# Kernel optimization log

Measured on AMD Instinct MI355X. Metric: run time of the kernel, lower is better.

The kernel has to match this reference:

```python
import jax, jax.numpy as jnp
import numpy as np

CHANNELS = 256
C8 = CHANNELS // 8


def setup_inputs() -> dict:
    key = jax.random.key(0)
    ks = jax.random.split(key, 7)
    b, c, h, w = 4, CHANNELS, 64, 64
    x = jax.random.normal(ks[0], (b, c, h, w), dtype=jnp.float32)
    # 1x1 conv weights stored as [out_ch, in_ch] (kernel is 1x1)
    s = 1.0 / np.sqrt(c)
    wq = jax.random.uniform(ks[1], (C8, c), jnp.float32, -s, s)
    bq = jax.random.uniform(ks[2], (C8,), jnp.float32, -s, s)
    wk = jax.random.uniform(ks[3], (C8, c), jnp.float32, -s, s)
    bk = jax.random.uniform(ks[4], (C8,), jnp.float32, -s, s)
    wv = jax.random.uniform(ks[5], (c, c), jnp.float32, -s, s)
    bv = jax.random.uniform(ks[6], (c,), jnp.float32, -s, s)
    return {"x": x, "wq": wq, "bq": bq, "wk": wk, "bk": bk, "wv": wv, "bv": bv}


def reference(x, wq, bq, wk, bk, wv, bv):
    b, c, h, w = x.shape
    n = h * w
    xf = x.reshape(b, c, n)                                  # (b, c, n)
    q = jnp.einsum('oc,bcn->bon', wq, xf) + bq[None, :, None]  # (b, c/8, n)
    k = jnp.einsum('oc,bcn->bon', wk, xf) + bk[None, :, None]  # (b, c/8, n)
    v = jnp.einsum('oc,bcn->bon', wv, xf) + bv[None, :, None]  # (b, c, n)
    # attention[b, i, j] = softmax_j( q[:, :, i] . k[:, :, j] )
    scores = jnp.einsum('bdi,bdj->bij', q, k)                # (b, n, n)
    attn = jax.nn.softmax(scores, axis=-1)
    # out = value @ attention^T  -> out[b, c, i] = sum_j v[b, c, j] * attn[b, i, j]
    out = jnp.einsum('bcj,bij->bci', v, attn)                # (b, c, n)
    return out.reshape(b, c, h, w) + x
```

## Files before the change

### kernel.cpp

```cpp
#include <hip/hip_runtime.h>
#include <hip/hip_bf16.h>
#include <stdint.h>

#define CH 256
#define D8 32
#define NN 4096

typedef __attribute__((ext_vector_type(8))) short short8;
typedef __attribute__((ext_vector_type(4))) short s16x4;
typedef __attribute__((ext_vector_type(4))) float f32x4;

#define MFMA16(a,b,c) __builtin_amdgcn_mfma_f32_16x16x32_bf16(a,b,c,0,0,0)

static __device__ __forceinline__ short f2bf(float f) {
  union { float f; uint32_t u; } v; v.f = f;
  uint32_t r = v.u + 0x7fffu + ((v.u >> 16) & 1u);
  return (short)(r >> 16);
}
static __device__ __forceinline__ float bf2f(short h) {
  union { float f; uint32_t u; } v; v.u = ((uint32_t)(uint16_t)h) << 16;
  return v.f;
}

__global__ __launch_bounds__(256) void prep_kernel(
    const float* __restrict__ x,
    const float* __restrict__ wq, const float* __restrict__ bq,
    const float* __restrict__ wk, const float* __restrict__ bk,
    const float* __restrict__ wv, const float* __restrict__ bv,
    short* __restrict__ xT, short* __restrict__ WQb,
    short* __restrict__ WKb, short* __restrict__ WVb,
    float* __restrict__ BQ, float* __restrict__ BK, float* __restrict__ BV)
{
  int blk = blockIdx.x, t = threadIdx.x;
  if (blk >= 1024) {
    int idx = (blk - 1024) * 256 + t;
    const float LOG2E = 1.4426950408889634f;
    for (int i = idx; i < D8 * CH; i += 2048) WQb[i] = f2bf(wq[i] * LOG2E);
    for (int i = idx; i < D8 * CH; i += 2048) WKb[i] = f2bf(wk[i]);
    for (int i = idx; i < CH * CH; i += 2048) WVb[i] = f2bf(wv[i]);
    if (idx < D8) { BQ[idx] = bq[idx] * LOG2E; BK[idx] = bk[idx]; }
    if (idx < CH) BV[idx] = bv[idx];
    return;
  }
  int b = blk >> 8, ct = (blk >> 6) & 3, nt = blk & 63;
  __shared__ short T[64][65];
  int j = t & 63, i0 = t >> 6;
  const float* xb = x + ((size_t)b * CH + ct * 64) * NN + nt * 64;
  #pragma unroll
  for (int k = 0; k < 16; ++k) {
    int i = k * 4 + i0;
    T[i][j] = f2bf(xb[(size_t)i * NN + j]);
  }
  __syncthreads();
  short* xTb = xT + ((size_t)b * NN + nt * 64) * CH + ct * 64;
  #pragma unroll
  for (int k = 0; k < 16; ++k) {
    int n = k * 4 + i0;
    xTb[(size_t)n * CH + j] = T[j][n];
  }
}

__global__ __launch_bounds__(256) void proj_kernel(
    const short* __restrict__ xT,
    const short* __restrict__ WQb, const short* __restrict__ WKb,
    const short* __restrict__ WVb,
    const float* __restrict__ BQ, const float* __restrict__ BK,
    const float* __restrict__ BV,
    short* __restrict__ Qh, short* __restrict__ Ql,
    short* __restrict__ Kh, short* __restrict__ Kl,
    short* __restrict__ Vo)
{
  int blk = blockIdx.x, t = threadIdx.x;
  int b = blk >> 8, pt = blk & 255;
  int w = t >> 6, lane = t & 63, g = lane >> 4, lr = lane & 15;
  int p0 = pt * 16;
  __shared__ short Vt[4][16][20];

  const short* xrow = xT + ((size_t)b * NN + p0 + lr) * CH + g * 8;
  short8 a[8];
  #pragma unroll
  for (int s = 0; s < 8; ++s) a[s] = *(const short8*)(xrow + s * 32);

  const f32x4 zf = {0.f, 0.f, 0.f, 0.f};

  #pragma unroll
  for (int i = 0; i < 5; ++i) {
    int tt = w * 5 + i;
    const short* W; const float* Bs; int tloc;
    if (tt < 2)      { W = WQb; Bs = BQ; tloc = tt; }
    else if (tt < 4) { W = WKb; Bs = BK; tloc = tt - 2; }
    else             { W = WVb; Bs = BV; tloc = tt - 4; }
    f32x4 acc = zf;
    #pragma unroll
    for (int s = 0; s < 8; ++s) {
      short8 bb = *(const short8*)(W + (size_t)(tloc * 16 + lr) * CH + s * 32 + g * 8);
      acc = MFMA16(a[s], bb, acc);
    }
    int o = tloc * 16 + lr;
    float bias = Bs[o];
    if (tt < 4) {
      short* Oh = (tt < 2) ? Qh : Kh;
      short* Ol = (tt < 2) ? Ql : Kl;
      #pragma unroll
      for (int r = 0; r < 4; ++r) {
        int pos = p0 + g * 4 + r;
        float val = acc[r] + bias;
        short hi = f2bf(val);
        Oh[((size_t)b * NN + pos) * D8 + o] = hi;
        Ol[((size_t)b * NN + pos) * D8 + o] = f2bf(val - bf2f(hi));
      }
    } else {
      #pragma unroll
      for (int r = 0; r < 4; ++r)
        Vt[w][lr][g * 4 + r] = f2bf(acc[r] + bias);
      int row = lane >> 2, c4 = (lane & 3) * 4;
      s16x4 vv = *(const s16x4*)&Vt[w][row][c4];
      *(s16x4*)(Vo + ((size_t)b * CH + tloc * 16 + row) * NN + p0 + c4) = vv;
    }
  }
}

__global__ __launch_bounds__(512) void attn_kernel(
    const short* __restrict__ Qh, const short* __restrict__ Ql,
    const short* __restrict__ Kh, const short* __restrict__ Kl,
    const short* __restrict__ V, const float* __restrict__ x,
    float* __restrict__ out)
{
  int blk = blockIdx.x, t = threadIdx.x;
  int xcd = blk & 7, idx = blk >> 3;
  int b = xcd >> 1;
  int qt = ((xcd & 1) << 5) + idx;
  int q0 = qt * 64;
  int w = t >> 6, lane = t & 63, g = lane >> 4, lr = lane & 15;
  int wS = w & 3;
  bool isS = (w < 4);
  int cw0 = w * 32;

  union Smem {
    struct {
      short P[2][64 * 64];
      float scale[2][64];
      int   flags[2][4];
    } lp;
    float O[CH][67];
  };
  __shared__ Smem sm;
  __shared__ float l_lds[64];

  const short* Qhb = Qh + (size_t)b * NN * D8;
  const short* Qlb = Ql + (size_t)b * NN * D8;
  const short* Khb = Kh + (size_t)b * NN * D8;
  const short* Klb = Kl + (size_t)b * NN * D8;
  const short* Vb = V + (size_t)b * CH * NN;

  short8 aqh, aql;
  if (isS) {
    aqh = *(const short8*)(Qhb + (size_t)(q0 + wS * 16 + lr) * D8 + g * 8);
    aql = *(const short8*)(Qlb + (size_t)(q0 + wS * 16 + lr) * D8 + g * 8);
  }

  const f32x4 zf = {0.f, 0.f, 0.f, 0.f};
  f32x4 O[4][2];
  #pragma unroll
  for (int i = 0; i < 4; ++i)
    #pragma unroll
    for (int j = 0; j < 2; ++j) O[i][j] = zf;
  float m[4] = {-INFINITY, -INFINITY, -INFINITY, -INFINITY};
  float l[4] = {0.f, 0.f, 0.f, 0.f};

  char* Pbase0 = (char*)&sm.lp.P[0][0];
  char* Pbase1 = (char*)&sm.lp.P[1][0];

#define LOADK(KH, KL, KIDX) do { \
    int _k0 = (KIDX) * 64; \
    _Pragma("unroll") \
    for (int _nt = 0; _nt < 4; ++_nt) { \
      size_t _off = (size_t)(_k0 + _nt * 16 + lr) * D8 + g * 8; \
      KH[_nt] = *(const short8*)(Khb + _off); \
      KL[_nt] = *(const short8*)(Klb + _off); \
    } \
  } while (0)

#define LOADV(VV, KIDX) do { \
    int _k0 = (KIDX) * 64; \
    _Pragma("unroll") \
    for (int _ss = 0; _ss < 2; ++_ss) \
      _Pragma("unroll") \
      for (int _ci = 0; _ci < 2; ++_ci) \
        VV[_ss * 2 + _ci] = *(const short8*)(Vb + \
            (size_t)(cw0 + _ci * 16 + lr) * NN + _k0 + _ss * 32 + g * 8); \
  } while (0)

#define STEP(KB, KH, KL, VV, NKH, NKL, NVV) do { \
    int _buf = (KB) & 1; \
    char* _Pb = _buf ? Pbase1 : Pbase0; \
    int _kn = ((KB) + 1) & 63; \
    if (isS) { \
       \
      f32x4 S[4]; \
      _Pragma("unroll") \
      for (int nt = 0; nt < 4; ++nt) { \
        f32x4 s_ = MFMA16(aql, KH[nt], zf); \
        s_ = MFMA16(aqh, KL[nt], s_); \
        s_ = MFMA16(aqh, KH[nt], s_); \
        S[nt] = s_; \
      } \
      LOADK(NKH, NKL, _kn); \
      LOADV(NVV, _kn); \
       \
      float sc[4]; \
      bool upd = false; \
      _Pragma("unroll") \
      for (int r = 0; r < 4; ++r) { \
        float v = fmaxf(fmaxf(S[0][r], S[1][r]), fmaxf(S[2][r], S[3][r])); \
        v = fmaxf(v, __shfl_xor(v, 1)); \
        v = fmaxf(v, __shfl_xor(v, 2)); \
        v = fmaxf(v, __shfl_xor(v, 4)); \
        v = fmaxf(v, __shfl_xor(v, 8)); \
        bool u = v > m[r] + 8.0f;                 \
        upd |= u; \
        float mn = u ? v : m[r]; \
        sc[r] = __builtin_amdgcn_exp2f(m[r] - mn); \
        m[r] = mn; \
      } \
      bool anyupd = __any((int)upd); \
      float rsum[4] = {0.f, 0.f, 0.f, 0.f}; \
      short pb[4][4]; \
      _Pragma("unroll") \
      for (int nt = 0; nt < 4; ++nt) \
        _Pragma("unroll") \
        for (int r = 0; r < 4; ++r) { \
          float p = __builtin_amdgcn_exp2f(S[nt][r] - m[r]); \
          rsum[r] += p; \
          pb[nt][r] = f2bf(p); \
        } \
      _Pragma("unroll") \
      for (int r = 0; r < 4; ++r) { \
        float v = rsum[r]; \
        v += __shfl_xor(v, 1); v += __shfl_xor(v, 2); \
        v += __shfl_xor(v, 4); v += __shfl_xor(v, 8); \
        l[r] = l[r] * sc[r] + v; \
      } \
       \
      _Pragma("unroll") \
      for (int nt = 0; nt < 4; ++nt) \
        _Pragma("unroll") \
        for (int r = 0; r < 4; ++r) { \
          int qloc = wS * 16 + g * 4 + r; \
          int kk = nt * 16 + lr; \
          int off = (qloc * 128 + kk * 2) ^ ((qloc & 7) << 4); \
          *(short*)(_Pb + off) = pb[nt][r]; \
        } \
      if (lr == 0) { \
        _Pragma("unroll") \
        for (int r = 0; r < 4; ++r) \
          sm.lp.scale[_buf][wS * 16 + g * 4 + r] = sc[r]; \
      } \
      if (lane == 0) sm.lp.flags[_buf][wS] = anyupd ? 1 : 0; \
    } else { \
      LOADV(NVV, _kn); \
    } \
    __syncthreads();                              \
    int need = sm.lp.flags[_buf][0] | sm.lp.flags[_buf][1] | \
               sm.lp.flags[_buf][2] | sm.lp.flags[_buf][3]; \
    if (need) { \
      _Pragma("unroll") \
      for (int mi = 0; mi < 4; ++mi) \
        _Pragma("unroll") \
        for (int r = 0; r < 4; ++r) { \
          float s = sm.lp.scale[_buf][mi * 16 + g * 4 + r]; \
          _Pragma("unroll") \
          for (int ci = 0; ci < 2; ++ci) O[mi][ci][r] *= s; \
        } \
    } \
     \
    __builtin_amdgcn_s_setprio(1); \
    _Pragma("unroll") \
    for (int ss = 0; ss < 2; ++ss) { \
      short8 ap[4]; \
      _Pragma("unroll") \
      for (int mi = 0; mi < 4; ++mi) { \
        int row = mi * 16 + lr; \
        int off = (row * 128 + (ss * 32 + g * 8) * 2) ^ ((row & 7) << 4); \
        ap[mi] = *(const short8*)(_Pb + off); \
      } \
      _Pragma("unroll") \
      for (int ci = 0; ci < 2; ++ci) { \
        _Pragma("unroll") \
        for (int mi = 0; mi < 4; ++mi) \
          O[mi][ci] = MFMA16(ap[mi], VV[ss * 2 + ci], O[mi][ci]); \
      } \
    } \
    __builtin_amdgcn_s_setprio(0); \
  } while (0)

  short8 khA[4], klA[4], vA[4], khB[4], klB[4], vB[4];
  if (isS) LOADK(khA, klA, 0);
  LOADV(vA, 0);
  #pragma unroll 1
  for (int kb2 = 0; kb2 < 32; ++kb2) {
    STEP(2 * kb2,     khA, klA, vA, khB, klB, vB);
    STEP(2 * kb2 + 1, khB, klB, vB, khA, klA, vA);
  }
#undef STEP
#undef LOADK
#undef LOADV

  if (isS && lr == 0) {
    #pragma unroll
    for (int r = 0; r < 4; ++r)
      l_lds[wS * 16 + g * 4 + r] = l[r];
  }
  __syncthreads();
  #pragma unroll
  for (int mi = 0; mi < 4; ++mi)
    #pragma unroll
    for (int ci = 0; ci < 2; ++ci) {
      int ch = cw0 + ci * 16 + lr;
      #pragma unroll
      for (int r = 0; r < 4; ++r)
        sm.O[ch][mi * 16 + g * 4 + r] = O[mi][ci][r];
    }
  __syncthreads();
  int q = t & 63, crow = t >> 6;
  float linv = 1.0f / l_lds[q];
  const float* xb = x + (size_t)b * CH * NN + q0 + q;
  float* ob = out + (size_t)b * CH * NN + q0 + q;
  #pragma unroll
  for (int oi = 0; oi < 32; ++oi) {
    int ch = crow * 32 + oi;
    ob[(size_t)ch * NN] = sm.O[ch][q] * linv + xb[(size_t)ch * NN];
  }
}

extern "C" void kernel_launch(void* const* d_in, const int* in_sizes, int n_in,
                              void* d_out, int out_size, void* d_ws, size_t ws_size,
                              hipStream_t stream) {
  const float* x  = (const float*)d_in[0];
  const float* wq = (const float*)d_in[1];
  const float* bq = (const float*)d_in[2];
  const float* wk = (const float*)d_in[3];
  const float* bk = (const float*)d_in[4];
  const float* wv = (const float*)d_in[5];
  const float* bv = (const float*)d_in[6];
  char* ws = (char*)d_ws;
  short* xT  = (short*)(ws);
  short* Qh  = (short*)(ws + 8388608);
  short* Ql  = (short*)(ws + 9437184);
  short* Kh  = (short*)(ws + 10485760);
  short* Kl  = (short*)(ws + 11534336);
  short* Vo  = (short*)(ws + 12582912);
  short* WQb = (short*)(ws + 20971520);
  short* WKb = (short*)(ws + 20987904);
  short* WVb = (short*)(ws + 21004288);
  float* BQ  = (float*)(ws + 21135360);
  float* BK  = (float*)(ws + 21135488);
  float* BV  = (float*)(ws + 21135616);

  prep_kernel<<<1032, 256, 0, stream>>>(x, wq, bq, wk, bk, wv, bv,
                                        xT, WQb, WKb, WVb, BQ, BK, BV);
  proj_kernel<<<1024, 256, 0, stream>>>(xT, WQb, WKb, WVb, BQ, BK, BV,
                                        Qh, Ql, Kh, Kl, Vo);
  attn_kernel<<<256, 512, 0, stream>>>(Qh, Ql, Kh, Kl, Vo, x, (float*)d_out);
}
```

Measured before the change: 218.3 us.

## Specialize attention waves into softmax producers and PV consumers with software pipelining

The attention kernel now splits its waves by role. Four waves compute QK scores and the softmax, and the other four compute the P·V MFMAs over all 256 channels (64 each) one key block behind, so the two stages overlap across barriers. The change also replaces shuffle reductions with DPP row reductions and double-buffers the weight loads in the projection kernel. In exchange, the PV waves hold twice the accumulator registers, and the pipeline adds one extra stage at the end.

```diff
diff --git a/kernel.cpp b/kernel.cpp
--- a/kernel.cpp
+++ b/kernel.cpp
@@ -21,6 +21,25 @@
   union { float f; uint32_t u; } v; v.u = ((uint32_t)(uint16_t)h) << 16;
   return v.f;
 }
+static __device__ __forceinline__ int f2i(float f) {
+  union { float f; int i; } v; v.f = f; return v.i;
+}
+static __device__ __forceinline__ float i2f(int i) {
+  union { float f; int i; } v; v.i = i; return v.f;
+}
+
+#define DPP_MAX16(V) do { \
+    V = fmaxf(V, i2f(__builtin_amdgcn_update_dpp(0, f2i(V), 0xB1, 0xf, 0xf, true)));  \
+    V = fmaxf(V, i2f(__builtin_amdgcn_update_dpp(0, f2i(V), 0x4E, 0xf, 0xf, true)));  \
+    V = fmaxf(V, i2f(__builtin_amdgcn_update_dpp(0, f2i(V), 0x124, 0xf, 0xf, true))); \
+    V = fmaxf(V, i2f(__builtin_amdgcn_update_dpp(0, f2i(V), 0x128, 0xf, 0xf, true))); \
+  } while (0)
+#define DPP_SUM16(V) do { \
+    V += i2f(__builtin_amdgcn_update_dpp(0, f2i(V), 0xB1, 0xf, 0xf, true));  \
+    V += i2f(__builtin_amdgcn_update_dpp(0, f2i(V), 0x4E, 0xf, 0xf, true));  \
+    V += i2f(__builtin_amdgcn_update_dpp(0, f2i(V), 0x124, 0xf, 0xf, true)); \
+    V += i2f(__builtin_amdgcn_update_dpp(0, f2i(V), 0x128, 0xf, 0xf, true)); \
+  } while (0)
 
 __global__ __launch_bounds__(256) void prep_kernel(
     const float* __restrict__ x,
@@ -83,41 +102,57 @@
 
   const f32x4 zf = {0.f, 0.f, 0.f, 0.f};
 
-  #pragma unroll
-  for (int i = 0; i < 5; ++i) {
-    int tt = w * 5 + i;
-    const short* W; const float* Bs; int tloc;
-    if (tt < 2)      { W = WQb; Bs = BQ; tloc = tt; }
-    else if (tt < 4) { W = WKb; Bs = BK; tloc = tt - 2; }
-    else             { W = WVb; Bs = BV; tloc = tt - 4; }
-    f32x4 acc = zf;
-    #pragma unroll
-    for (int s = 0; s < 8; ++s) {
-      short8 bb = *(const short8*)(W + (size_t)(tloc * 16 + lr) * CH + s * 32 + g * 8);
-      acc = MFMA16(a[s], bb, acc);
-    }
-    int o = tloc * 16 + lr;
-    float bias = Bs[o];
-    if (tt < 4) {
-      short* Oh = (tt < 2) ? Qh : Kh;
-      short* Ol = (tt < 2) ? Ql : Kl;
-      #pragma unroll
-      for (int r = 0; r < 4; ++r) {
-        int pos = p0 + g * 4 + r;
-        float val = acc[r] + bias;
-        short hi = f2bf(val);
-        Oh[((size_t)b * NN + pos) * D8 + o] = hi;
-        Ol[((size_t)b * NN + pos) * D8 + o] = f2bf(val - bf2f(hi));
-      }
-    } else {
-      #pragma unroll
-      for (int r = 0; r < 4; ++r)
-        Vt[w][lr][g * 4 + r] = f2bf(acc[r] + bias);
-      int row = lane >> 2, c4 = (lane & 3) * 4;
-      s16x4 vv = *(const s16x4*)&Vt[w][row][c4];
-      *(s16x4*)(Vo + ((size_t)b * CH + tloc * 16 + row) * NN + p0 + c4) = vv;
-    }
-  }
+#define WLOAD(DST, TT) do { \
+    const short* _W; int _tl; \
+    if ((TT) < 2)      { _W = WQb; _tl = (TT); } \
+    else if ((TT) < 4) { _W = WKb; _tl = (TT) - 2; } \
+    else               { _W = WVb; _tl = (TT) - 4; } \
+    _Pragma("unroll") \
+    for (int s = 0; s < 8; ++s) \
+      DST[s] = *(const short8*)(_W + (size_t)(_tl * 16 + lr) * CH + s * 32 + g * 8); \
+  } while (0)
+
+#define WCOMP(CUR, TT) do { \
+    int _tloc; const float* _Bs; \
+    if ((TT) < 2)      { _Bs = BQ; _tloc = (TT); } \
+    else if ((TT) < 4) { _Bs = BK; _tloc = (TT) - 2; } \
+    else               { _Bs = BV; _tloc = (TT) - 4; } \
+    f32x4 acc = zf; \
+    _Pragma("unroll") \
+    for (int s = 0; s < 8; ++s) acc = MFMA16(a[s], CUR[s], acc); \
+    int o = _tloc * 16 + lr; \
+    float bias = _Bs[o]; \
+    if ((TT) < 4) { \
+      short* Oh = ((TT) < 2) ? Qh : Kh; \
+      short* Ol = ((TT) < 2) ? Ql : Kl; \
+      _Pragma("unroll") \
+      for (int r = 0; r < 4; ++r) { \
+        int pos = p0 + g * 4 + r; \
+        float val = acc[r] + bias; \
+        short hi = f2bf(val); \
+        Oh[((size_t)b * NN + pos) * D8 + o] = hi; \
+        Ol[((size_t)b * NN + pos) * D8 + o] = f2bf(val - bf2f(hi)); \
+      } \
+    } else { \
+      _Pragma("unroll") \
+      for (int r = 0; r < 4; ++r) \
+        Vt[w][lr][g * 4 + r] = f2bf(acc[r] + bias); \
+      int row = lane >> 2, c4 = (lane & 3) * 4; \
+      s16x4 vv = *(const s16x4*)&Vt[w][row][c4]; \
+      *(s16x4*)(Vo + ((size_t)b * CH + _tloc * 16 + row) * NN + p0 + c4) = vv; \
+    } \
+  } while (0)
+
+  int t0 = w * 5;
+  short8 bA[8], bB[8];
+  WLOAD(bA, t0);
+  WLOAD(bB, t0 + 1); WCOMP(bA, t0);
+  WLOAD(bA, t0 + 2); WCOMP(bB, t0 + 1);
+  WLOAD(bB, t0 + 3); WCOMP(bA, t0 + 2);
+  WLOAD(bA, t0 + 4); WCOMP(bB, t0 + 3);
+  WCOMP(bA, t0 + 4);
+#undef WLOAD
+#undef WCOMP
 }
 
 __global__ __launch_bounds__(512) void attn_kernel(
@@ -134,7 +169,7 @@
   int w = t >> 6, lane = t & 63, g = lane >> 4, lr = lane & 15;
   int wS = w & 3;
   bool isS = (w < 4);
-  int cw0 = w * 32;
+  int cw0 = wS * 64;
 
   union Smem {
     struct {
@@ -160,11 +195,11 @@
   }
 
   const f32x4 zf = {0.f, 0.f, 0.f, 0.f};
-  f32x4 O[4][2];
+  f32x4 O[4][4];
   #pragma unroll
   for (int i = 0; i < 4; ++i)
     #pragma unroll
-    for (int j = 0; j < 2; ++j) O[i][j] = zf;
+    for (int j = 0; j < 4; ++j) O[i][j] = zf;
   float m[4] = {-INFINITY, -INFINITY, -INFINITY, -INFINITY};
   float l[4] = {0.f, 0.f, 0.f, 0.f};
 
@@ -181,99 +216,86 @@
     } \
   } while (0)
 
-#define LOADV(VV, KIDX) do { \
-    int _k0 = (KIDX) * 64; \
+#define SSTEP(KB, KH, KL, NKH, NKL, PBASE, PAR) do { \
+    f32x4 S[4]; \
+    _Pragma("unroll") \
+    for (int nt = 0; nt < 4; ++nt) { \
+      f32x4 s_ = MFMA16(aql, KH[nt], zf); \
+      s_ = MFMA16(aqh, KL[nt], s_); \
+      s_ = MFMA16(aqh, KH[nt], s_); \
+      S[nt] = s_; \
+    } \
+    LOADK(NKH, NKL, ((KB) + 1) & 63); \
+    float sc[4]; \
+    bool upd = false; \
+    _Pragma("unroll") \
+    for (int r = 0; r < 4; ++r) { \
+      float v = fmaxf(fmaxf(S[0][r], S[1][r]), fmaxf(S[2][r], S[3][r])); \
+      DPP_MAX16(v); \
+      bool u = v > m[r] + 8.0f;                   \
+      upd |= u; \
+      float mn = u ? v : m[r]; \
+      sc[r] = __builtin_amdgcn_exp2f(m[r] - mn); \
+      m[r] = mn; \
+    } \
+    bool anyupd = __any((int)upd); \
+    short pb[4][4]; \
+    float rsum[4]; \
+    _Pragma("unroll") \
+    for (int r = 0; r < 4; ++r) { \
+      float acc = 0.f; \
+      _Pragma("unroll") \
+      for (int nt = 0; nt < 4; ++nt) { \
+        float p = __builtin_amdgcn_exp2f(S[nt][r] - m[r]); \
+        acc += p; \
+        pb[nt][r] = f2bf(p); \
+      } \
+      rsum[r] = acc; \
+    } \
+    _Pragma("unroll") \
+    for (int r = 0; r < 4; ++r) { \
+      float v = rsum[r]; \
+      DPP_SUM16(v); \
+      l[r] = l[r] * sc[r] + v; \
+    } \
+    _Pragma("unroll") \
+    for (int nt = 0; nt < 4; ++nt) \
+      _Pragma("unroll") \
+      for (int r = 0; r < 4; ++r) { \
+        int qloc = wS * 16 + g * 4 + r; \
+        int kk = nt * 16 + lr; \
+        int off = (qloc * 128 + kk * 2) ^ ((qloc & 7) << 4); \
+        *(short*)((PBASE) + off) = pb[nt][r]; \
+      } \
+    if (lr == 0) { \
+      _Pragma("unroll") \
+      for (int r = 0; r < 4; ++r) \
+        sm.lp.scale[PAR][wS * 16 + g * 4 + r] = sc[r]; \
+    } \
+    if (lane == 0) sm.lp.flags[PAR][wS] = anyupd ? 1 : 0; \
+  } while (0)
+
+#define PSTEP(CPREV, PBASE, PAR) do { \
+    short8 vv[8]; \
+    int _k0 = (CPREV) * 64; \
     _Pragma("unroll") \
     for (int _ss = 0; _ss < 2; ++_ss) \
       _Pragma("unroll") \
-      for (int _ci = 0; _ci < 2; ++_ci) \
-        VV[_ss * 2 + _ci] = *(const short8*)(Vb + \
+      for (int _ci = 0; _ci < 4; ++_ci) \
+        vv[_ss * 4 + _ci] = *(const short8*)(Vb + \
             (size_t)(cw0 + _ci * 16 + lr) * NN + _k0 + _ss * 32 + g * 8); \
-  } while (0)
-
-#define STEP(KB, KH, KL, VV, NKH, NKL, NVV) do { \
-    int _buf = (KB) & 1; \
-    char* _Pb = _buf ? Pbase1 : Pbase0; \
-    int _kn = ((KB) + 1) & 63; \
-    if (isS) { \
-       \
-      f32x4 S[4]; \
-      _Pragma("unroll") \
-      for (int nt = 0; nt < 4; ++nt) { \
-        f32x4 s_ = MFMA16(aql, KH[nt], zf); \
-        s_ = MFMA16(aqh, KL[nt], s_); \
-        s_ = MFMA16(aqh, KH[nt], s_); \
-        S[nt] = s_; \
-      } \
-      LOADK(NKH, NKL, _kn); \
-      LOADV(NVV, _kn); \
-       \
-      float sc[4]; \
-      bool upd = false; \
-      _Pragma("unroll") \
-      for (int r = 0; r < 4; ++r) { \
-        float v = fmaxf(fmaxf(S[0][r], S[1][r]), fmaxf(S[2][r], S[3][r])); \
-        v = fmaxf(v, __shfl_xor(v, 1)); \
-        v = fmaxf(v, __shfl_xor(v, 2)); \
-        v = fmaxf(v, __shfl_xor(v, 4)); \
-        v = fmaxf(v, __shfl_xor(v, 8)); \
-        bool u = v > m[r] + 8.0f;                 \
-        upd |= u; \
-        float mn = u ? v : m[r]; \
-        sc[r] = __builtin_amdgcn_exp2f(m[r] - mn); \
-        m[r] = mn; \
-      } \
-      bool anyupd = __any((int)upd); \
-      float rsum[4] = {0.f, 0.f, 0.f, 0.f}; \
-      short pb[4][4]; \
-      _Pragma("unroll") \
-      for (int nt = 0; nt < 4; ++nt) \
-        _Pragma("unroll") \
-        for (int r = 0; r < 4; ++r) { \
-          float p = __builtin_amdgcn_exp2f(S[nt][r] - m[r]); \
-          rsum[r] += p; \
-          pb[nt][r] = f2bf(p); \
-        } \
-      _Pragma("unroll") \
-      for (int r = 0; r < 4; ++r) { \
-        float v = rsum[r]; \
-        v += __shfl_xor(v, 1); v += __shfl_xor(v, 2); \
-        v += __shfl_xor(v, 4); v += __shfl_xor(v, 8); \
-        l[r] = l[r] * sc[r] + v; \
-      } \
-       \
-      _Pragma("unroll") \
-      for (int nt = 0; nt < 4; ++nt) \
-        _Pragma("unroll") \
-        for (int r = 0; r < 4; ++r) { \
-          int qloc = wS * 16 + g * 4 + r; \
-          int kk = nt * 16 + lr; \
-          int off = (qloc * 128 + kk * 2) ^ ((qloc & 7) << 4); \
-          *(short*)(_Pb + off) = pb[nt][r]; \
-        } \
-      if (lr == 0) { \
-        _Pragma("unroll") \
-        for (int r = 0; r < 4; ++r) \
-          sm.lp.scale[_buf][wS * 16 + g * 4 + r] = sc[r]; \
-      } \
-      if (lane == 0) sm.lp.flags[_buf][wS] = anyupd ? 1 : 0; \
-    } else { \
-      LOADV(NVV, _kn); \
-    } \
-    __syncthreads();                              \
-    int need = sm.lp.flags[_buf][0] | sm.lp.flags[_buf][1] | \
-               sm.lp.flags[_buf][2] | sm.lp.flags[_buf][3]; \
+    int need = sm.lp.flags[PAR][0] | sm.lp.flags[PAR][1] | \
+               sm.lp.flags[PAR][2] | sm.lp.flags[PAR][3]; \
     if (need) { \
       _Pragma("unroll") \
       for (int mi = 0; mi < 4; ++mi) \
         _Pragma("unroll") \
         for (int r = 0; r < 4; ++r) { \
-          float s = sm.lp.scale[_buf][mi * 16 + g * 4 + r]; \
+          float s = sm.lp.scale[PAR][mi * 16 + g * 4 + r]; \
           _Pragma("unroll") \
-          for (int ci = 0; ci < 2; ++ci) O[mi][ci][r] *= s; \
+          for (int ci = 0; ci < 4; ++ci) O[mi][ci][r] *= s; \
         } \
     } \
-     \
     __builtin_amdgcn_s_setprio(1); \
     _Pragma("unroll") \
     for (int ss = 0; ss < 2; ++ss) { \
@@ -282,45 +304,55 @@
       for (int mi = 0; mi < 4; ++mi) { \
         int row = mi * 16 + lr; \
         int off = (row * 128 + (ss * 32 + g * 8) * 2) ^ ((row & 7) << 4); \
-        ap[mi] = *(const short8*)(_Pb + off); \
-      } \
-      _Pragma("unroll") \
-      for (int ci = 0; ci < 2; ++ci) { \
+        ap[mi] = *(const short8*)((PBASE) + off); \
+      } \
+      _Pragma("unroll") \
+      for (int ci = 0; ci < 4; ++ci) { \
         _Pragma("unroll") \
         for (int mi = 0; mi < 4; ++mi) \
-          O[mi][ci] = MFMA16(ap[mi], VV[ss * 2 + ci], O[mi][ci]); \
+          O[mi][ci] = MFMA16(ap[mi], vv[ss * 4 + ci], O[mi][ci]); \
       } \
     } \
     __builtin_amdgcn_s_setprio(0); \
   } while (0)
 
-  short8 khA[4], klA[4], vA[4], khB[4], klB[4], vB[4];
+  short8 khA[4], klA[4], khB[4], klB[4];
   if (isS) LOADK(khA, klA, 0);
-  LOADV(vA, 0);
   #pragma unroll 1
   for (int kb2 = 0; kb2 < 32; ++kb2) {
-    STEP(2 * kb2,     khA, klA, vA, khB, klB, vB);
-    STEP(2 * kb2 + 1, khB, klB, vB, khA, klA, vA);
-  }
-#undef STEP
+    int ke = 2 * kb2;
+    if (isS)            SSTEP(ke, khA, klA, khB, klB, Pbase0, 0);
+    else if (ke > 0)    PSTEP(ke - 1, Pbase1, 1);
+    __syncthreads();
+    if (isS)            SSTEP(ke + 1, khB, klB, khA, klA, Pbase1, 1);
+    else                PSTEP(ke, Pbase0, 0);
+    __syncthreads();
+  }
+#undef SSTEP
 #undef LOADK
-#undef LOADV
-
-  if (isS && lr == 0) {
-    #pragma unroll
-    for (int r = 0; r < 4; ++r)
-      l_lds[wS * 16 + g * 4 + r] = l[r];
-  }
-  __syncthreads();
-  #pragma unroll
-  for (int mi = 0; mi < 4; ++mi)
-    #pragma unroll
-    for (int ci = 0; ci < 2; ++ci) {
-      int ch = cw0 + ci * 16 + lr;
+
+  if (isS) {
+    if (lr == 0) {
       #pragma unroll
       for (int r = 0; r < 4; ++r)
-        sm.O[ch][mi * 16 + g * 4 + r] = O[mi][ci][r];
+        l_lds[wS * 16 + g * 4 + r] = l[r];
     }
+  } else {
+    PSTEP(63, Pbase1, 1);
+  }
+#undef PSTEP
+  __syncthreads();
+  if (!isS) {
+    #pragma unroll
+    for (int mi = 0; mi < 4; ++mi)
+      #pragma unroll
+      for (int ci = 0; ci < 4; ++ci) {
+        int ch = cw0 + ci * 16 + lr;
+        #pragma unroll
+        for (int r = 0; r < 4; ++r)
+          sm.O[ch][mi * 16 + g * 4 + r] = O[mi][ci][r];
+      }
+  }
   __syncthreads();
   int q = t & 63, crow = t >> 6;
   float linv = 1.0f / l_lds[q];
```

Result: slower. 229.1 us (+4.9%).
